# Performance work log

Measured on AMD Instinct MI355X. Metric: run time of the kernel, lower is better.

The kernel has to match this reference:

```python
import jax, jax.numpy as jnp
import numpy as np

DIM = 2048
DIM_HEAD = 64
HEADS = 16
FF_MULT = 4
LORA_R = 8
ATTN_INNER = DIM_HEAD * HEADS            # 1024
FF_INNER = DIM * FF_MULT                 # 8192
FUSED_DIMS = (ATTN_INNER, DIM_HEAD, DIM_HEAD, FF_INNER * 2)
B, N = 2, 2048


def setup_inputs() -> dict:
    key = jax.random.key(0)
    ks = jax.random.split(key, 12)
    s = 0.02
    inp = {
        "x": jax.random.normal(ks[0], (B, N, DIM), dtype=jnp.float32),
        "gamma": jnp.ones((DIM,), dtype=jnp.float32),
        "w_fused": jax.random.normal(ks[1], (DIM, sum(FUSED_DIMS)), dtype=jnp.float32) * s,
        "w_attn_out": jax.random.normal(ks[2], (ATTN_INNER, DIM), dtype=jnp.float32) * s,
        "w_ff_out": jax.random.normal(ks[3], (FF_INNER, DIM), dtype=jnp.float32) * s,
        "lora_q_a": jax.random.normal(ks[4], (DIM, LORA_R), dtype=jnp.float32) * s,
        "lora_q_b": jax.random.normal(ks[5], (LORA_R, ATTN_INNER), dtype=jnp.float32) * s,
        "lora_k_a": jax.random.normal(ks[6], (DIM, LORA_R), dtype=jnp.float32) * s,
        "lora_k_b": jax.random.normal(ks[7], (LORA_R, DIM_HEAD), dtype=jnp.float32) * s,
        "lora_v_a": jax.random.normal(ks[8], (DIM, LORA_R), dtype=jnp.float32) * s,
        "lora_v_b": jax.random.normal(ks[9], (LORA_R, DIM_HEAD), dtype=jnp.float32) * s,
        "lora_o_a": jax.random.normal(ks[10], (ATTN_INNER, LORA_R), dtype=jnp.float32) * s,
        "lora_o_b": jax.random.normal(ks[11], (LORA_R, DIM), dtype=jnp.float32) * s,
    }
    return inp


def _rotate_half(x):
    x1, x2 = jnp.split(x, 2, axis=-1)
    return jnp.concatenate((-x2, x1), axis=-1)


def _rope(pos, t):
    return t * jnp.cos(pos) + _rotate_half(t) * jnp.sin(pos)


def _forward(x, gamma, w_fused, w_attn_out, w_ff_out,
             lora_q_a, lora_q_b, lora_k_a, lora_k_b,
             lora_v_a, lora_v_b, lora_o_a, lora_o_b):
    b, n, d = x.shape
    # LayerNorm (beta = 0)
    mu = jnp.mean(x, axis=-1, keepdims=True)
    var = jnp.var(x, axis=-1, keepdims=True)
    xn = (x - mu) * jax.lax.rsqrt(var + 1e-5) * gamma

    fused = xn @ w_fused
    i0, i1, i2 = np.cumsum(FUSED_DIMS)[:3]
    q, k, v, ff = fused[..., :i0], fused[..., i0:i1], fused[..., i1:i2], fused[..., i2:]

    # LoRA additive terms
    q = q + (xn @ lora_q_a) @ lora_q_b
    k = k + (xn @ lora_k_a) @ lora_k_b
    v = v + (xn @ lora_v_a) @ lora_v_b

    q = q.reshape(b, n, HEADS, DIM_HEAD).transpose(0, 2, 1, 3)  # b h n d
    q = q * (DIM_HEAD ** -0.5)

    # rotary embedding: pos (n, dim_head)
    inv_freq = 1.0 / (10000.0 ** (jnp.arange(0, DIM_HEAD, 2, dtype=jnp.float32) / DIM_HEAD))
    freqs = jnp.arange(n, dtype=jnp.float32)[:, None] * inv_freq[None, :]
    pos = jnp.concatenate((freqs, freqs), axis=-1)
    q = _rope(pos, q)
    k = _rope(pos, k)  # k is b n d (multi-query, single kv head)

    sim = jnp.einsum('bhid,bjd->bhij', q, k)
    causal = jnp.triu(jnp.ones((n, n), dtype=bool), k=1)
    sim = jnp.where(causal, -jnp.finfo(sim.dtype).max, sim)
    attn = jax.nn.softmax(sim, axis=-1)
    out = jnp.einsum('bhij,bjd->bhid', attn, v)
    out = out.transpose(0, 2, 1, 3).reshape(b, n, ATTN_INNER)

    attn_out = out @ w_attn_out + (out @ lora_o_a) @ lora_o_b

    # SwiGLU: chunk -> (x_ff, gate); silu(gate) * x_ff
    x_ff, gate = jnp.split(ff, 2, axis=-1)
    ff_out = (jax.nn.silu(gate) * x_ff) @ w_ff_out

    return attn_out + ff_out


def reference(x, gamma, w_fused, w_attn_out, w_ff_out,
              lora_q_a, lora_q_b, lora_k_a, lora_k_b,
              lora_v_a, lora_v_b, lora_o_a, lora_o_b):
    return _forward(x, gamma, w_fused, w_attn_out, w_ff_out,
                    lora_q_a, lora_q_b, lora_k_a, lora_k_b,
                    lora_v_a, lora_v_b, lora_o_a, lora_o_b)
```

## Files before the change

kernel.cpp:

```cpp
#include <hip/hip_runtime.h>
#include <cstdint>


typedef __bf16 bf16_t;
typedef __bf16 bf16x8 __attribute__((ext_vector_type(8)));
typedef float f32x4 __attribute__((ext_vector_type(4)));

#define LOG2E 1.44269504088896340736f
#define LOG2_10K 13.287712379549449f

__device__ __forceinline__ void gload_lds16(const void* g, void* l) {
  __builtin_amdgcn_global_load_lds(
      (__attribute__((address_space(1))) void*)(uintptr_t)g,
      (__attribute__((address_space(3))) void*)(uint32_t)(uintptr_t)l,
      16, 0, 0);
}

__device__ __forceinline__ f32x4 mfma16(bf16x8 a, bf16x8 b, f32x4 c) {
  return __builtin_amdgcn_mfma_f32_16x16x32_bf16(a, b, c, 0, 0, 0);
}

__global__ __launch_bounds__(256) void ln_kernel(
    const float* __restrict__ x, const float* __restrict__ gamma,
    bf16_t* __restrict__ xn)
{
  const int row = blockIdx.x;
  const int t = threadIdx.x;
  const float4* xr = (const float4*)(x + (size_t)row * 2048);
  float4 a = xr[t * 2];
  float4 b = xr[t * 2 + 1];
  float s  = a.x + a.y + a.z + a.w + b.x + b.y + b.z + b.w;
  float ss = a.x*a.x + a.y*a.y + a.z*a.z + a.w*a.w
           + b.x*b.x + b.y*b.y + b.z*b.z + b.w*b.w;
  #pragma unroll
  for (int m = 1; m < 64; m <<= 1) {
    s  += __shfl_xor(s, m);
    ss += __shfl_xor(ss, m);
  }
  __shared__ float red[8];
  const int wave = t >> 6, lane = t & 63;
  if (lane == 0) { red[wave] = s; red[4 + wave] = ss; }
  __syncthreads();
  const float stot  = red[0] + red[1] + red[2] + red[3];
  const float sstot = red[4] + red[5] + red[6] + red[7];
  const float mu  = stot * (1.f / 2048.f);
  const float var = sstot * (1.f / 2048.f) - mu * mu;
  const float rs  = rsqrtf(var + 1e-5f);
  float v[8] = {a.x, a.y, a.z, a.w, b.x, b.y, b.z, b.w};
  bf16x8 o;
  #pragma unroll
  for (int e = 0; e < 8; ++e)
    o[e] = (bf16_t)((v[e] - mu) * rs * gamma[t * 8 + e]);
  *(bf16x8*)(xn + (size_t)row * 2048 + t * 8) = o;
}

__global__ __launch_bounds__(256) void transpose_wf_kernel(
    const float* __restrict__ w,
    const float* __restrict__ qa, const float* __restrict__ qb,
    const float* __restrict__ ka, const float* __restrict__ kb,
    const float* __restrict__ va, const float* __restrict__ vb,
    bf16_t* __restrict__ wfT)
{
  __shared__ float tile[64][65];
  const int t  = threadIdx.x;
  const int n0 = blockIdx.x * 64;
  const int k0 = blockIdx.y * 64;
  #pragma unroll
  for (int it = 0; it < 4; ++it) {
    const int kr = (t >> 4) + it * 16;
    const float4 vv = *(const float4*)(w + (size_t)(k0 + kr) * 17536 + n0 + (t & 15) * 4);
    tile[kr][(t & 15) * 4 + 0] = vv.x;
    tile[kr][(t & 15) * 4 + 1] = vv.y;
    tile[kr][(t & 15) * 4 + 2] = vv.z;
    tile[kr][(t & 15) * 4 + 3] = vv.w;
  }
  __syncthreads();
  const float* la = nullptr; const float* lb = nullptr;
  int nbo = 0, ldlb = 0;
  if (n0 < 1024)      { la = qa; lb = qb; nbo = n0;        ldlb = 1024; }
  else if (n0 < 1088) { la = ka; lb = kb; nbo = n0 - 1024; ldlb = 64;   }
  else if (n0 < 1152) { la = va; lb = vb; nbo = n0 - 1088; ldlb = 64;   }
  #pragma unroll
  for (int it = 0; it < 2; ++it) {
    const int nl = (t >> 3) + it * 32;
    const int kl = (t & 7) * 8;
    float vals[8];
    #pragma unroll
    for (int e = 0; e < 8; ++e) vals[e] = tile[kl + e][nl];
    if (la) {
      float bc[8];
      #pragma unroll
      for (int r = 0; r < 8; ++r) bc[r] = lb[r * ldlb + nbo + nl];
      #pragma unroll
      for (int e = 0; e < 8; ++e) {
        const float* ar = la + (size_t)(k0 + kl + e) * 8;
        float d = 0.f;
        #pragma unroll
        for (int r = 0; r < 8; ++r) d += ar[r] * bc[r];
        vals[e] += d;
      }
    }
    bf16x8 o;
    #pragma unroll
    for (int e = 0; e < 8; ++e) o[e] = (bf16_t)vals[e];
    *(bf16x8*)(wfT + (size_t)(n0 + nl) * 2048 + k0 + kl) = o;
  }
}

__global__ __launch_bounds__(256) void transpose_w2_kernel(
    const float* __restrict__ wff,
    const float* __restrict__ watt,
    const float* __restrict__ oa, const float* __restrict__ ob,
    bf16_t* __restrict__ w2T)
{
  __shared__ float tile[64][65];
  const int t  = threadIdx.x;
  const int n0 = blockIdx.x * 64;
  const int k0 = blockIdx.y * 64;
  const bool isatt = (k0 >= 8192);
  const float* src = isatt ? (watt + (size_t)(k0 - 8192) * 2048)
                           : (wff + (size_t)k0 * 2048);
  #pragma unroll
  for (int it = 0; it < 4; ++it) {
    const int kr = (t >> 4) + it * 16;
    const float4 vv = *(const float4*)(src + (size_t)kr * 2048 + n0 + (t & 15) * 4);
    tile[kr][(t & 15) * 4 + 0] = vv.x;
    tile[kr][(t & 15) * 4 + 1] = vv.y;
    tile[kr][(t & 15) * 4 + 2] = vv.z;
    tile[kr][(t & 15) * 4 + 3] = vv.w;
  }
  __syncthreads();
  #pragma unroll
  for (int it = 0; it < 2; ++it) {
    const int nl = (t >> 3) + it * 32;
    const int kl = (t & 7) * 8;
    float vals[8];
    #pragma unroll
    for (int e = 0; e < 8; ++e) vals[e] = tile[kl + e][nl];
    if (isatt) {
      float bc[8];
      #pragma unroll
      for (int r = 0; r < 8; ++r) bc[r] = ob[r * 2048 + n0 + nl];
      #pragma unroll
      for (int e = 0; e < 8; ++e) {
        const float* ar = oa + (size_t)(k0 - 8192 + kl + e) * 8;
        float d = 0.f;
        #pragma unroll
        for (int r = 0; r < 8; ++r) d += ar[r] * bc[r];
        vals[e] += d;
      }
    }
    bf16x8 o;
    #pragma unroll
    for (int e = 0; e < 8; ++e) o[e] = (bf16_t)vals[e];
    *(bf16x8*)(w2T + (size_t)(n0 + nl) * 9216 + k0 + kl) = o;
  }
}

__device__ __forceinline__ void gemm_core_128x128(
    const bf16_t* __restrict__ A, int ldA, int m0,
    const bf16_t* __restrict__ BT, int ldB, int n0,
    int K, bf16_t* As, bf16_t* Bs, f32x4* acc)
{
  const int t = threadIdx.x;
  const int wave = t >> 6;
  const int lane = t & 63;
  const int quad = lane >> 4;
  const int ln15 = lane & 15;
  const int wm = wave & 1, wn = wave >> 1;

  const bf16_t* gA = A + (size_t)(m0 + (t >> 2)) * ldA + ((t & 3) << 3);
  const bf16_t* gB = BT + (size_t)(n0 + (t >> 2)) * ldB + ((t & 3) << 3);
  char* lA = (char*)As + wave * 1024;
  char* lB = (char*)Bs + wave * 1024;
  const size_t sA64 = (size_t)64 * ldA;
  const size_t sB64 = (size_t)64 * ldB;
  const int aoff = (wm * 64 + ln15) * 32 + quad * 8;
  const int boff = (wn * 64 + ln15) * 32 + quad * 8;

  for (int kt = 0; kt < K; kt += 32) {
    gload_lds16(gA,        lA);
    gload_lds16(gA + sA64, lA + 4096);
    gload_lds16(gB,        lB);
    gload_lds16(gB + sB64, lB + 4096);
    gA += 32;
    gB += 32;
    __syncthreads();
    bf16x8 a0 = *(const bf16x8*)(As + aoff);
    bf16x8 a1 = *(const bf16x8*)(As + aoff + 512);
    bf16x8 a2 = *(const bf16x8*)(As + aoff + 1024);
    bf16x8 a3 = *(const bf16x8*)(As + aoff + 1536);
    bf16x8 b0 = *(const bf16x8*)(Bs + boff);
    bf16x8 b1 = *(const bf16x8*)(Bs + boff + 512);
    bf16x8 b2 = *(const bf16x8*)(Bs + boff + 1024);
    bf16x8 b3 = *(const bf16x8*)(Bs + boff + 1536);
    acc[0]  = mfma16(a0, b0, acc[0]);
    acc[1]  = mfma16(a0, b1, acc[1]);
    acc[2]  = mfma16(a0, b2, acc[2]);
    acc[3]  = mfma16(a0, b3, acc[3]);
    acc[4]  = mfma16(a1, b0, acc[4]);
    acc[5]  = mfma16(a1, b1, acc[5]);
    acc[6]  = mfma16(a1, b2, acc[6]);
    acc[7]  = mfma16(a1, b3, acc[7]);
    acc[8]  = mfma16(a2, b0, acc[8]);
    acc[9]  = mfma16(a2, b1, acc[9]);
    acc[10] = mfma16(a2, b2, acc[10]);
    acc[11] = mfma16(a2, b3, acc[11]);
    acc[12] = mfma16(a3, b0, acc[12]);
    acc[13] = mfma16(a3, b1, acc[13]);
    acc[14] = mfma16(a3, b2, acc[14]);
    acc[15] = mfma16(a3, b3, acc[15]);
    __syncthreads();
  }
}

__global__ __launch_bounds__(256) void gemm1_qkv_kernel(
    const bf16_t* __restrict__ xn, const bf16_t* __restrict__ wfT,
    bf16_t* __restrict__ Q, bf16_t* __restrict__ K, bf16_t* __restrict__ Vt)
{
  __shared__ __align__(16) bf16_t As[128 * 32];
  __shared__ __align__(16) bf16_t Bs[128 * 32];
  const int m0 = blockIdx.x * 128;
  const int ct = blockIdx.y;
  const int t = threadIdx.x;
  const int wave = t >> 6, lane = t & 63;
  const int quad = lane >> 4, ln15 = lane & 15;
  const int wm = wave & 1, wn = wave >> 1;

  f32x4 acc[16];
  #pragma unroll
  for (int f = 0; f < 16; ++f) acc[f] = (f32x4){0.f, 0.f, 0.f, 0.f};
  gemm_core_128x128(xn, 2048, m0, wfT, 2048, ct * 128, 2048, As, Bs, acc);

  const int rb = m0 + wm * 64 + quad * 4;
  const bool is_k = (ct == 8) && (wn == 0);
  const bool is_v = (ct == 8) && (wn == 1);
  const float invf0 = exp2f(-(float)ln15 * (LOG2_10K / 32.0f));
  const float invf1 = exp2f(-(float)(16 + ln15) * (LOG2_10K / 32.0f));
  const int hd = ct * 2 + wn;

  #pragma unroll
  for (int i = 0; i < 4; ++i) {
    #pragma unroll
    for (int rr = 0; rr < 4; ++rr) {
      const int row = rb + i * 16 + rr;
      const int b = row >> 11, n = row & 2047;
      float vals[4];
      #pragma unroll
      for (int j = 0; j < 4; ++j) vals[j] = acc[i * 4 + j][rr];
      if (is_v) {
        #pragma unroll
        for (int j = 0; j < 4; ++j)
          Vt[((size_t)b * 64 + j * 16 + ln15) * 2048 + n] = (bf16_t)vals[j];
      } else {
        const float fn = (float)n;
        float s0, c0, s1, c1;
        __sincosf(fn * invf0, &s0, &c0);
        __sincosf(fn * invf1, &s1, &c1);
        #pragma unroll
        for (int j = 0; j < 4; ++j) {
          const float rot = (j < 2) ? -vals[j + 2] : vals[j - 2];
          const float c = (j & 1) ? c1 : c0;
          const float s = (j & 1) ? s1 : s0;
          const float o = vals[j] * c + rot * s;
          const int d = j * 16 + ln15;
          if (is_k)
            K[((size_t)b * 2048 + n) * 64 + d] = (bf16_t)o;
          else
            Q[(((size_t)b * 16 + hd) * 2048 + n) * 64 + d] = (bf16_t)(o * 0.125f);
        }
      }
    }
  }
}

__global__ __launch_bounds__(256, 2) void gemm1_ff_kernel(
    const bf16_t* __restrict__ xn, const bf16_t* __restrict__ wfT,
    bf16_t* __restrict__ A2)
{
  __shared__ __align__(16) bf16_t As[128 * 32];
  __shared__ __align__(16) bf16_t Bg[128 * 32];
  __shared__ __align__(16) bf16_t Bx[128 * 32];
  const int m0 = blockIdx.x * 128;
  const int c  = blockIdx.y;
  const int t = threadIdx.x;
  const int wave = t >> 6, lane = t & 63;
  const int quad = lane >> 4, ln15 = lane & 15;
  const int wm = wave & 1, wn = wave >> 1;

  const bf16_t* gA = xn  + (size_t)(m0 + (t >> 2)) * 2048 + ((t & 3) << 3);
  const bf16_t* gG = wfT + (size_t)(9344 + c * 128 + (t >> 2)) * 2048 + ((t & 3) << 3);
  const bf16_t* gX = wfT + (size_t)(1152 + c * 128 + (t >> 2)) * 2048 + ((t & 3) << 3);
  char* lA = (char*)As + wave * 1024;
  char* lG = (char*)Bg + wave * 1024;
  char* lX = (char*)Bx + wave * 1024;
  const size_t s64 = (size_t)64 * 2048;
  const int aoff = (wm * 64 + ln15) * 32 + quad * 8;
  const int boff = (wn * 64 + ln15) * 32 + quad * 8;

  f32x4 accg[16], accx[16];
  #pragma unroll
  for (int f = 0; f < 16; ++f) {
    accg[f] = (f32x4){0.f, 0.f, 0.f, 0.f};
    accx[f] = (f32x4){0.f, 0.f, 0.f, 0.f};
  }

  for (int kt = 0; kt < 2048; kt += 32) {
    gload_lds16(gA,       lA);
    gload_lds16(gA + s64, lA + 4096);
    gload_lds16(gG,       lG);
    gload_lds16(gG + s64, lG + 4096);
    gload_lds16(gX,       lX);
    gload_lds16(gX + s64, lX + 4096);
    gA += 32; gG += 32; gX += 32;
    __syncthreads();
    bf16x8 a0 = *(const bf16x8*)(As + aoff);
    bf16x8 a1 = *(const bf16x8*)(As + aoff + 512);
    bf16x8 a2 = *(const bf16x8*)(As + aoff + 1024);
    bf16x8 a3 = *(const bf16x8*)(As + aoff + 1536);
    bf16x8 g0 = *(const bf16x8*)(Bg + boff);
    bf16x8 g1 = *(const bf16x8*)(Bg + boff + 512);
    bf16x8 g2 = *(const bf16x8*)(Bg + boff + 1024);
    bf16x8 g3 = *(const bf16x8*)(Bg + boff + 1536);
    bf16x8 x0 = *(const bf16x8*)(Bx + boff);
    bf16x8 x1 = *(const bf16x8*)(Bx + boff + 512);
    bf16x8 x2 = *(const bf16x8*)(Bx + boff + 1024);
    bf16x8 x3 = *(const bf16x8*)(Bx + boff + 1536);
    accg[0]  = mfma16(a0, g0, accg[0]);
    accg[1]  = mfma16(a0, g1, accg[1]);
    accg[2]  = mfma16(a0, g2, accg[2]);
    accg[3]  = mfma16(a0, g3, accg[3]);
    accx[0]  = mfma16(a0, x0, accx[0]);
    accx[1]  = mfma16(a0, x1, accx[1]);
    accx[2]  = mfma16(a0, x2, accx[2]);
    accx[3]  = mfma16(a0, x3, accx[3]);
    accg[4]  = mfma16(a1, g0, accg[4]);
    accg[5]  = mfma16(a1, g1, accg[5]);
    accg[6]  = mfma16(a1, g2, accg[6]);
    accg[7]  = mfma16(a1, g3, accg[7]);
    accx[4]  = mfma16(a1, x0, accx[4]);
    accx[5]  = mfma16(a1, x1, accx[5]);
    accx[6]  = mfma16(a1, x2, accx[6]);
    accx[7]  = mfma16(a1, x3, accx[7]);
    accg[8]  = mfma16(a2, g0, accg[8]);
    accg[9]  = mfma16(a2, g1, accg[9]);
    accg[10] = mfma16(a2, g2, accg[10]);
    accg[11] = mfma16(a2, g3, accg[11]);
    accx[8]  = mfma16(a2, x0, accx[8]);
    accx[9]  = mfma16(a2, x1, accx[9]);
    accx[10] = mfma16(a2, x2, accx[10]);
    accx[11] = mfma16(a2, x3, accx[11]);
    accg[12] = mfma16(a3, g0, accg[12]);
    accg[13] = mfma16(a3, g1, accg[13]);
    accg[14] = mfma16(a3, g2, accg[14]);
    accg[15] = mfma16(a3, g3, accg[15]);
    accx[12] = mfma16(a3, x0, accx[12]);
    accx[13] = mfma16(a3, x1, accx[13]);
    accx[14] = mfma16(a3, x2, accx[14]);
    accx[15] = mfma16(a3, x3, accx[15]);
    __syncthreads();
  }

  const int rb = m0 + wm * 64 + quad * 4;
  const int cb = c * 128 + wn * 64 + ln15;
  #pragma unroll
  for (int i = 0; i < 4; ++i)
    #pragma unroll
    for (int rr = 0; rr < 4; ++rr) {
      bf16_t* dst = A2 + (size_t)(rb + i * 16 + rr) * 9216 + cb;
      #pragma unroll
      for (int j = 0; j < 4; ++j) {
        const float g = accg[i * 4 + j][rr];
        const float xv = accx[i * 4 + j][rr];
        dst[j * 16] = (bf16_t)(xv * (g / (1.f + exp2f(-g * LOG2E))));
      }
    }
}

__global__ __launch_bounds__(256, 2) void gemm2_kernel(
    const bf16_t* __restrict__ A2, const bf16_t* __restrict__ w2T,
    float* __restrict__ out)
{
  __shared__ __align__(16) bf16_t As[128 * 32];
  __shared__ __align__(16) bf16_t B0[128 * 32];
  __shared__ __align__(16) bf16_t B1[128 * 32];
  const int m0 = blockIdx.x * 128;
  const int n0 = blockIdx.y * 256;
  const int k0 = blockIdx.z * 4608;
  const int t = threadIdx.x;
  const int wave = t >> 6, lane = t & 63;
  const int quad = lane >> 4, ln15 = lane & 15;
  const int wm = wave & 1, wn = wave >> 1;

  const bf16_t* gA  = A2  + (size_t)(m0 + (t >> 2)) * 9216 + k0 + ((t & 3) << 3);
  const bf16_t* gB0 = w2T + (size_t)(n0 + (t >> 2)) * 9216 + k0 + ((t & 3) << 3);
  const bf16_t* gB1 = w2T + (size_t)(n0 + 128 + (t >> 2)) * 9216 + k0 + ((t & 3) << 3);
  char* lA = (char*)As + wave * 1024;
  char* l0 = (char*)B0 + wave * 1024;
  char* l1 = (char*)B1 + wave * 1024;
  const size_t s64 = (size_t)64 * 9216;
  const int aoff = (wm * 64 + ln15) * 32 + quad * 8;
  const int boff = (wn * 64 + ln15) * 32 + quad * 8;

  f32x4 acc0[16], acc1[16];
  #pragma unroll
  for (int f = 0; f < 16; ++f) {
    acc0[f] = (f32x4){0.f, 0.f, 0.f, 0.f};
    acc1[f] = (f32x4){0.f, 0.f, 0.f, 0.f};
  }

  for (int kt = 0; kt < 4608; kt += 32) {
    gload_lds16(gA,        lA);
    gload_lds16(gA + s64,  lA + 4096);
    gload_lds16(gB0,       l0);
    gload_lds16(gB0 + s64, l0 + 4096);
    gload_lds16(gB1,       l1);
    gload_lds16(gB1 + s64, l1 + 4096);
    gA += 32; gB0 += 32; gB1 += 32;
    __syncthreads();
    bf16x8 a0 = *(const bf16x8*)(As + aoff);
    bf16x8 a1 = *(const bf16x8*)(As + aoff + 512);
    bf16x8 a2 = *(const bf16x8*)(As + aoff + 1024);
    bf16x8 a3 = *(const bf16x8*)(As + aoff + 1536);
    bf16x8 p0 = *(const bf16x8*)(B0 + boff);
    bf16x8 p1 = *(const bf16x8*)(B0 + boff + 512);
    bf16x8 p2 = *(const bf16x8*)(B0 + boff + 1024);
    bf16x8 p3 = *(const bf16x8*)(B0 + boff + 1536);
    bf16x8 q0 = *(const bf16x8*)(B1 + boff);
    bf16x8 q1 = *(const bf16x8*)(B1 + boff + 512);
    bf16x8 q2 = *(const bf16x8*)(B1 + boff + 1024);
    bf16x8 q3 = *(const bf16x8*)(B1 + boff + 1536);
    acc0[0]  = mfma16(a0, p0, acc0[0]);
    acc0[1]  = mfma16(a0, p1, acc0[1]);
    acc0[2]  = mfma16(a0, p2, acc0[2]);
    acc0[3]  = mfma16(a0, p3, acc0[3]);
    acc1[0]  = mfma16(a0, q0, acc1[0]);
    acc1[1]  = mfma16(a0, q1, acc1[1]);
    acc1[2]  = mfma16(a0, q2, acc1[2]);
    acc1[3]  = mfma16(a0, q3, acc1[3]);
    acc0[4]  = mfma16(a1, p0, acc0[4]);
    acc0[5]  = mfma16(a1, p1, acc0[5]);
    acc0[6]  = mfma16(a1, p2, acc0[6]);
    acc0[7]  = mfma16(a1, p3, acc0[7]);
    acc1[4]  = mfma16(a1, q0, acc1[4]);
    acc1[5]  = mfma16(a1, q1, acc1[5]);
    acc1[6]  = mfma16(a1, q2, acc1[6]);
    acc1[7]  = mfma16(a1, q3, acc1[7]);
    acc0[8]  = mfma16(a2, p0, acc0[8]);
    acc0[9]  = mfma16(a2, p1, acc0[9]);
    acc0[10] = mfma16(a2, p2, acc0[10]);
    acc0[11] = mfma16(a2, p3, acc0[11]);
    acc1[8]  = mfma16(a2, q0, acc1[8]);
    acc1[9]  = mfma16(a2, q1, acc1[9]);
    acc1[10] = mfma16(a2, q2, acc1[10]);
    acc1[11] = mfma16(a2, q3, acc1[11]);
    acc0[12] = mfma16(a3, p0, acc0[12]);
    acc0[13] = mfma16(a3, p1, acc0[13]);
    acc0[14] = mfma16(a3, p2, acc0[14]);
    acc0[15] = mfma16(a3, p3, acc0[15]);
    acc1[12] = mfma16(a3, q0, acc1[12]);
    acc1[13] = mfma16(a3, q1, acc1[13]);
    acc1[14] = mfma16(a3, q2, acc1[14]);
    acc1[15] = mfma16(a3, q3, acc1[15]);
    __syncthreads();
  }

  const int rb = m0 + wm * 64 + quad * 4;
  #pragma unroll
  for (int half = 0; half < 2; ++half) {
    const f32x4* acc = half ? acc1 : acc0;
    const int cb = n0 + half * 128 + wn * 64 + ln15;
    #pragma unroll
    for (int i = 0; i < 4; ++i)
      #pragma unroll
      for (int rr = 0; rr < 4; ++rr) {
        float* dst = out + (size_t)(rb + i * 16 + rr) * 2048 + cb;
        #pragma unroll
        for (int j = 0; j < 4; ++j)
          unsafeAtomicAdd(dst + j * 16, acc[i * 4 + j][rr]);
      }
  }
}

__global__ __launch_bounds__(256) void attn_kernel(
    const bf16_t* __restrict__ Q, const bf16_t* __restrict__ Kg_,
    const bf16_t* __restrict__ Vt, bf16_t* __restrict__ A2)
{
  __shared__ __align__(16) bf16_t Qs[128 * 64];
  __shared__ __align__(16) bf16_t Ks[64 * 64];
  __shared__ __align__(16) bf16_t Vs[64 * 64];
  __shared__ __align__(16) bf16_t Ps[128 * 64];
  const int pidx = blockIdx.x, bh = blockIdx.y;
  const int b = bh >> 4, h = bh & 15;
  const int t = threadIdx.x;
  const int wave = t >> 6, lane = t & 63;
  const int quad = lane >> 4, ln15 = lane & 15;

  const bf16_t* Kg = Kg_ + (size_t)b * 2048 * 64;
  const bf16_t* Vg = Vt + (size_t)b * 64 * 2048;

  for (int hlf = 0; hlf < 2; ++hlf) {
    const int qt = hlf ? (15 - pidx) : pidx;
    const int qm0 = qt * 128;
    const bf16_t* Qg = Q + ((size_t)bh * 2048 + qm0) * 64;

    {
      const bf16_t* g = Qg + (size_t)(t >> 3) * 64 + ((t & 7) << 3);
      char* l = (char*)Qs + wave * 1024;
      gload_lds16(g,            l);
      gload_lds16(g + 32 * 64,  l + 4096);
      gload_lds16(g + 64 * 64,  l + 8192);
      gload_lds16(g + 96 * 64,  l + 12288);
    }

    float mstate[2][4], lstate[2][4];
    f32x4 o_acc[2][4];
    #pragma unroll
    for (int i = 0; i < 2; ++i)
      #pragma unroll
      for (int rr = 0; rr < 4; ++rr) { mstate[i][rr] = -1e30f; lstate[i][rr] = 0.f; }
    #pragma unroll
    for (int i = 0; i < 2; ++i)
      #pragma unroll
      for (int jd = 0; jd < 4; ++jd) o_acc[i][jd] = (f32x4){0.f, 0.f, 0.f, 0.f};

    const int njt = qt * 2 + 2;
    for (int jt = 0; jt < njt; ++jt) {
      {
        const bf16_t* kg = Kg + (size_t)(jt * 64 + (t >> 3)) * 64 + ((t & 7) << 3);
        char* lk = (char*)Ks + wave * 1024;
        gload_lds16(kg,           lk);
        gload_lds16(kg + 32 * 64, lk + 4096);
        const bf16_t* vg = Vg + (size_t)(t >> 3) * 2048 + jt * 64 + ((t & 7) << 3);
        char* lv = (char*)Vs + wave * 1024;
        gload_lds16(vg,                   lv);
        gload_lds16(vg + (size_t)32*2048, lv + 4096);
      }
      __syncthreads();

      f32x4 sA[2][4];
      #pragma unroll
      for (int i = 0; i < 2; ++i)
        #pragma unroll
        for (int j = 0; j < 4; ++j) sA[i][j] = (f32x4){0.f, 0.f, 0.f, 0.f};
      #pragma unroll
      for (int ks = 0; ks < 2; ++ks) {
        bf16x8 aq0 = *(const bf16x8*)(Qs + (wave * 32 + ln15) * 64 + ks * 32 + quad * 8);
        bf16x8 aq1 = *(const bf16x8*)(Qs + (wave * 32 + 16 + ln15) * 64 + ks * 32 + quad * 8);
        #pragma unroll
        for (int j = 0; j < 4; ++j) {
          bf16x8 bk = *(const bf16x8*)(Ks + (j * 16 + ln15) * 64 + ks * 32 + quad * 8);
          sA[0][j] = mfma16(aq0, bk, sA[0][j]);
          sA[1][j] = mfma16(aq1, bk, sA[1][j]);
        }
      }

      const bool needmask = (jt * 64 + 63 > qm0 + wave * 32);
      #pragma unroll
      for (int i = 0; i < 2; ++i) {
        const int row0 = qm0 + wave * 32 + i * 16 + quad * 4;
        float alpha[4];
        #pragma unroll
        for (int rr = 0; rr < 4; ++rr) {
          const int rowg = row0 + rr;
          if (needmask) {
            #pragma unroll
            for (int j = 0; j < 4; ++j) {
              const int colg = jt * 64 + j * 16 + ln15;
              if (colg > rowg) sA[i][j][rr] = -1e30f;
            }
          }
          float mx = fmaxf(fmaxf(sA[i][0][rr], sA[i][1][rr]),
                           fmaxf(sA[i][2][rr], sA[i][3][rr]));
          mx = fmaxf(mx, __shfl_xor(mx, 1));
          mx = fmaxf(mx, __shfl_xor(mx, 2));
          mx = fmaxf(mx, __shfl_xor(mx, 4));
          mx = fmaxf(mx, __shfl_xor(mx, 8));
          const float mold = mstate[i][rr];
          const float mnew = fmaxf(mold, mx);
          const float al = exp2f((mold - mnew) * LOG2E);
          float rsum = 0.f;
          #pragma unroll
          for (int j = 0; j < 4; ++j) {
            const float p = exp2f((sA[i][j][rr] - mnew) * LOG2E);
            sA[i][j][rr] = p;
            rsum += p;
          }
          rsum += __shfl_xor(rsum, 1);
          rsum += __shfl_xor(rsum, 2);
          rsum += __shfl_xor(rsum, 4);
          rsum += __shfl_xor(rsum, 8);
          lstate[i][rr] = lstate[i][rr] * al + rsum;
          mstate[i][rr] = mnew;
          alpha[rr] = al;
        }
        #pragma unroll
        for (int jd = 0; jd < 4; ++jd)
          #pragma unroll
          for (int rr = 0; rr < 4; ++rr)
            o_acc[i][jd][rr] *= alpha[rr];
        #pragma unroll
        for (int j = 0; j < 4; ++j)
          #pragma unroll
          for (int rr = 0; rr < 4; ++rr)
            Ps[wave * 2048 + (i * 16 + quad * 4 + rr) * 64 + j * 16 + ln15] =
                (bf16_t)sA[i][j][rr];
      }

      #pragma unroll
      for (int ks = 0; ks < 2; ++ks) {
        bf16x8 ap0 = *(const bf16x8*)(Ps + wave * 2048 + ln15 * 64 + ks * 32 + quad * 8);
        bf16x8 ap1 = *(const bf16x8*)(Ps + wave * 2048 + (16 + ln15) * 64 + ks * 32 + quad * 8);
        #pragma unroll
        for (int jd = 0; jd < 4; ++jd) {
          bf16x8 bv = *(const bf16x8*)(Vs + (jd * 16 + ln15) * 64 + ks * 32 + quad * 8);
          o_acc[0][jd] = mfma16(ap0, bv, o_acc[0][jd]);
          o_acc[1][jd] = mfma16(ap1, bv, o_acc[1][jd]);
        }
      }
      __syncthreads();
    }

    #pragma unroll
    for (int i = 0; i < 2; ++i) {
      const int row0 = qm0 + wave * 32 + i * 16 + quad * 4;
      #pragma unroll
      for (int rr = 0; rr < 4; ++rr) {
        const float inv = 1.f / lstate[i][rr];
        bf16_t* dst = A2 + ((size_t)b * 2048 + row0 + rr) * 9216 + 8192 + h * 64 + ln15;
        #pragma unroll
        for (int jd = 0; jd < 4; ++jd)
          dst[jd * 16] = (bf16_t)(o_acc[i][jd][rr] * inv);
      }
    }
  }
}

extern "C" void kernel_launch(void* const* d_in, const int* in_sizes, int n_in,
                              void* d_out, int out_size, void* d_ws, size_t ws_size,
                              hipStream_t stream)
{
  const float* x      = (const float*)d_in[0];
  const float* gamma  = (const float*)d_in[1];
  const float* wfused = (const float*)d_in[2];
  const float* watt   = (const float*)d_in[3];
  const float* wff    = (const float*)d_in[4];
  const float* qa     = (const float*)d_in[5];
  const float* qb     = (const float*)d_in[6];
  const float* ka     = (const float*)d_in[7];
  const float* kb     = (const float*)d_in[8];
  const float* va     = (const float*)d_in[9];
  const float* vb     = (const float*)d_in[10];
  const float* oa     = (const float*)d_in[11];
  const float* ob     = (const float*)d_in[12];
  float* out = (float*)d_out;

  char* ws = (char*)d_ws;
  bf16_t* xn  = (bf16_t*)(ws);
  bf16_t* wfT = (bf16_t*)(ws + 16777216);
  bf16_t* w2T = (bf16_t*)(ws + 88604672);
  bf16_t* A2  = (bf16_t*)(ws + 126353408);
  bf16_t* Qr  = (bf16_t*)(ws + 201850880);
  bf16_t* Kr  = (bf16_t*)(ws + 210239488);
  bf16_t* Vtr = (bf16_t*)(ws + 210763776);

  hipMemsetAsync(d_out, 0, (size_t)out_size * sizeof(float), stream);

  ln_kernel<<<dim3(4096), dim3(256), 0, stream>>>(x, gamma, xn);
  transpose_wf_kernel<<<dim3(274, 32), dim3(256), 0, stream>>>(
      wfused, qa, qb, ka, kb, va, vb, wfT);
  transpose_w2_kernel<<<dim3(32, 144), dim3(256), 0, stream>>>(
      wff, watt, oa, ob, w2T);
  gemm1_qkv_kernel<<<dim3(32, 9), dim3(256), 0, stream>>>(xn, wfT, Qr, Kr, Vtr);
  gemm1_ff_kernel<<<dim3(32, 64), dim3(256), 0, stream>>>(xn, wfT, A2);
  attn_kernel<<<dim3(8, 32), dim3(256), 0, stream>>>(Qr, Kr, Vtr, A2);
  gemm2_kernel<<<dim3(32, 8, 2), dim3(256), 0, stream>>>(A2, w2T, out);
}
```

Baseline: 1.010 ms.

## Retile QKV GEMM to 128x256, shrink attention Q tile to 64, split FF launch

The Q projection blocks now compute 128x256 tiles through a shared dual-B GEMM core, cutting the QKV grid from 9 to 5 column blocks. K and V get a separate 128x128 path. The attention kernel drops from 128-row to 64-row query tiles with one 16-row slice per wave. That doubles the grid and halves LDS so two blocks can share a CU, which should improve occupancy and causal load balance. The FF GEMM is split into two launches over halves of M, and the duplicated GEMM loops are pulled into a single helper.

```diff
diff --git a/kernel.cpp b/kernel.cpp
--- a/kernel.cpp
+++ b/kernel.cpp
@@ -214,222 +214,48 @@
   }
 }
 
-__global__ __launch_bounds__(256) void gemm1_qkv_kernel(
-    const bf16_t* __restrict__ xn, const bf16_t* __restrict__ wfT,
-    bf16_t* __restrict__ Q, bf16_t* __restrict__ K, bf16_t* __restrict__ Vt)
-{
-  __shared__ __align__(16) bf16_t As[128 * 32];
-  __shared__ __align__(16) bf16_t Bs[128 * 32];
-  const int m0 = blockIdx.x * 128;
-  const int ct = blockIdx.y;
+__device__ __forceinline__ void gemm_core_dual(
+    const bf16_t* gA, const bf16_t* gB0, const bf16_t* gB1,
+    int ldA, int ldB, int K,
+    bf16_t* As, bf16_t* B0s, bf16_t* B1s,
+    f32x4* acc0, f32x4* acc1)
+{
   const int t = threadIdx.x;
-  const int wave = t >> 6, lane = t & 63;
-  const int quad = lane >> 4, ln15 = lane & 15;
+  const int wave = t >> 6;
+  const int lane = t & 63;
+  const int quad = lane >> 4;
+  const int ln15 = lane & 15;
   const int wm = wave & 1, wn = wave >> 1;
 
-  f32x4 acc[16];
-  #pragma unroll
-  for (int f = 0; f < 16; ++f) acc[f] = (f32x4){0.f, 0.f, 0.f, 0.f};
-  gemm_core_128x128(xn, 2048, m0, wfT, 2048, ct * 128, 2048, As, Bs, acc);
-
-  const int rb = m0 + wm * 64 + quad * 4;
-  const bool is_k = (ct == 8) && (wn == 0);
-  const bool is_v = (ct == 8) && (wn == 1);
-  const float invf0 = exp2f(-(float)ln15 * (LOG2_10K / 32.0f));
-  const float invf1 = exp2f(-(float)(16 + ln15) * (LOG2_10K / 32.0f));
-  const int hd = ct * 2 + wn;
-
-  #pragma unroll
-  for (int i = 0; i < 4; ++i) {
-    #pragma unroll
-    for (int rr = 0; rr < 4; ++rr) {
-      const int row = rb + i * 16 + rr;
-      const int b = row >> 11, n = row & 2047;
-      float vals[4];
-      #pragma unroll
-      for (int j = 0; j < 4; ++j) vals[j] = acc[i * 4 + j][rr];
-      if (is_v) {
-        #pragma unroll
-        for (int j = 0; j < 4; ++j)
-          Vt[((size_t)b * 64 + j * 16 + ln15) * 2048 + n] = (bf16_t)vals[j];
-      } else {
-        const float fn = (float)n;
-        float s0, c0, s1, c1;
-        __sincosf(fn * invf0, &s0, &c0);
-        __sincosf(fn * invf1, &s1, &c1);
-        #pragma unroll
-        for (int j = 0; j < 4; ++j) {
-          const float rot = (j < 2) ? -vals[j + 2] : vals[j - 2];
-          const float c = (j & 1) ? c1 : c0;
-          const float s = (j & 1) ? s1 : s0;
-          const float o = vals[j] * c + rot * s;
-          const int d = j * 16 + ln15;
-          if (is_k)
-            K[((size_t)b * 2048 + n) * 64 + d] = (bf16_t)o;
-          else
-            Q[(((size_t)b * 16 + hd) * 2048 + n) * 64 + d] = (bf16_t)(o * 0.125f);
-        }
-      }
-    }
-  }
-}
-
-__global__ __launch_bounds__(256, 2) void gemm1_ff_kernel(
-    const bf16_t* __restrict__ xn, const bf16_t* __restrict__ wfT,
-    bf16_t* __restrict__ A2)
-{
-  __shared__ __align__(16) bf16_t As[128 * 32];
-  __shared__ __align__(16) bf16_t Bg[128 * 32];
-  __shared__ __align__(16) bf16_t Bx[128 * 32];
-  const int m0 = blockIdx.x * 128;
-  const int c  = blockIdx.y;
-  const int t = threadIdx.x;
-  const int wave = t >> 6, lane = t & 63;
-  const int quad = lane >> 4, ln15 = lane & 15;
-  const int wm = wave & 1, wn = wave >> 1;
-
-  const bf16_t* gA = xn  + (size_t)(m0 + (t >> 2)) * 2048 + ((t & 3) << 3);
-  const bf16_t* gG = wfT + (size_t)(9344 + c * 128 + (t >> 2)) * 2048 + ((t & 3) << 3);
-  const bf16_t* gX = wfT + (size_t)(1152 + c * 128 + (t >> 2)) * 2048 + ((t & 3) << 3);
   char* lA = (char*)As + wave * 1024;
-  char* lG = (char*)Bg + wave * 1024;
-  char* lX = (char*)Bx + wave * 1024;
-  const size_t s64 = (size_t)64 * 2048;
+  char* l0 = (char*)B0s + wave * 1024;
+  char* l1 = (char*)B1s + wave * 1024;
+  const size_t sA64 = (size_t)64 * ldA;
+  const size_t sB64 = (size_t)64 * ldB;
   const int aoff = (wm * 64 + ln15) * 32 + quad * 8;
   const int boff = (wn * 64 + ln15) * 32 + quad * 8;
 
-  f32x4 accg[16], accx[16];
-  #pragma unroll
-  for (int f = 0; f < 16; ++f) {
-    accg[f] = (f32x4){0.f, 0.f, 0.f, 0.f};
-    accx[f] = (f32x4){0.f, 0.f, 0.f, 0.f};
-  }
-
-  for (int kt = 0; kt < 2048; kt += 32) {
-    gload_lds16(gA,       lA);
-    gload_lds16(gA + s64, lA + 4096);
-    gload_lds16(gG,       lG);
-    gload_lds16(gG + s64, lG + 4096);
-    gload_lds16(gX,       lX);
-    gload_lds16(gX + s64, lX + 4096);
-    gA += 32; gG += 32; gX += 32;
-    __syncthreads();
-    bf16x8 a0 = *(const bf16x8*)(As + aoff);
-    bf16x8 a1 = *(const bf16x8*)(As + aoff + 512);
-    bf16x8 a2 = *(const bf16x8*)(As + aoff + 1024);
-    bf16x8 a3 = *(const bf16x8*)(As + aoff + 1536);
-    bf16x8 g0 = *(const bf16x8*)(Bg + boff);
-    bf16x8 g1 = *(const bf16x8*)(Bg + boff + 512);
-    bf16x8 g2 = *(const bf16x8*)(Bg + boff + 1024);
-    bf16x8 g3 = *(const bf16x8*)(Bg + boff + 1536);
-    bf16x8 x0 = *(const bf16x8*)(Bx + boff);
-    bf16x8 x1 = *(const bf16x8*)(Bx + boff + 512);
-    bf16x8 x2 = *(const bf16x8*)(Bx + boff + 1024);
-    bf16x8 x3 = *(const bf16x8*)(Bx + boff + 1536);
-    accg[0]  = mfma16(a0, g0, accg[0]);
-    accg[1]  = mfma16(a0, g1, accg[1]);
-    accg[2]  = mfma16(a0, g2, accg[2]);
-    accg[3]  = mfma16(a0, g3, accg[3]);
-    accx[0]  = mfma16(a0, x0, accx[0]);
-    accx[1]  = mfma16(a0, x1, accx[1]);
-    accx[2]  = mfma16(a0, x2, accx[2]);
-    accx[3]  = mfma16(a0, x3, accx[3]);
-    accg[4]  = mfma16(a1, g0, accg[4]);
-    accg[5]  = mfma16(a1, g1, accg[5]);
-    accg[6]  = mfma16(a1, g2, accg[6]);
-    accg[7]  = mfma16(a1, g3, accg[7]);
-    accx[4]  = mfma16(a1, x0, accx[4]);
-    accx[5]  = mfma16(a1, x1, accx[5]);
-    accx[6]  = mfma16(a1, x2, accx[6]);
-    accx[7]  = mfma16(a1, x3, accx[7]);
-    accg[8]  = mfma16(a2, g0, accg[8]);
-    accg[9]  = mfma16(a2, g1, accg[9]);
-    accg[10] = mfma16(a2, g2, accg[10]);
-    accg[11] = mfma16(a2, g3, accg[11]);
-    accx[8]  = mfma16(a2, x0, accx[8]);
-    accx[9]  = mfma16(a2, x1, accx[9]);
-    accx[10] = mfma16(a2, x2, accx[10]);
-    accx[11] = mfma16(a2, x3, accx[11]);
-    accg[12] = mfma16(a3, g0, accg[12]);
-    accg[13] = mfma16(a3, g1, accg[13]);
-    accg[14] = mfma16(a3, g2, accg[14]);
-    accg[15] = mfma16(a3, g3, accg[15]);
-    accx[12] = mfma16(a3, x0, accx[12]);
-    accx[13] = mfma16(a3, x1, accx[13]);
-    accx[14] = mfma16(a3, x2, accx[14]);
-    accx[15] = mfma16(a3, x3, accx[15]);
-    __syncthreads();
-  }
-
-  const int rb = m0 + wm * 64 + quad * 4;
-  const int cb = c * 128 + wn * 64 + ln15;
-  #pragma unroll
-  for (int i = 0; i < 4; ++i)
-    #pragma unroll
-    for (int rr = 0; rr < 4; ++rr) {
-      bf16_t* dst = A2 + (size_t)(rb + i * 16 + rr) * 9216 + cb;
-      #pragma unroll
-      for (int j = 0; j < 4; ++j) {
-        const float g = accg[i * 4 + j][rr];
-        const float xv = accx[i * 4 + j][rr];
-        dst[j * 16] = (bf16_t)(xv * (g / (1.f + exp2f(-g * LOG2E))));
-      }
-    }
-}
-
-__global__ __launch_bounds__(256, 2) void gemm2_kernel(
-    const bf16_t* __restrict__ A2, const bf16_t* __restrict__ w2T,
-    float* __restrict__ out)
-{
-  __shared__ __align__(16) bf16_t As[128 * 32];
-  __shared__ __align__(16) bf16_t B0[128 * 32];
-  __shared__ __align__(16) bf16_t B1[128 * 32];
-  const int m0 = blockIdx.x * 128;
-  const int n0 = blockIdx.y * 256;
-  const int k0 = blockIdx.z * 4608;
-  const int t = threadIdx.x;
-  const int wave = t >> 6, lane = t & 63;
-  const int quad = lane >> 4, ln15 = lane & 15;
-  const int wm = wave & 1, wn = wave >> 1;
-
-  const bf16_t* gA  = A2  + (size_t)(m0 + (t >> 2)) * 9216 + k0 + ((t & 3) << 3);
-  const bf16_t* gB0 = w2T + (size_t)(n0 + (t >> 2)) * 9216 + k0 + ((t & 3) << 3);
-  const bf16_t* gB1 = w2T + (size_t)(n0 + 128 + (t >> 2)) * 9216 + k0 + ((t & 3) << 3);
-  char* lA = (char*)As + wave * 1024;
-  char* l0 = (char*)B0 + wave * 1024;
-  char* l1 = (char*)B1 + wave * 1024;
-  const size_t s64 = (size_t)64 * 9216;
-  const int aoff = (wm * 64 + ln15) * 32 + quad * 8;
-  const int boff = (wn * 64 + ln15) * 32 + quad * 8;
-
-  f32x4 acc0[16], acc1[16];
-  #pragma unroll
-  for (int f = 0; f < 16; ++f) {
-    acc0[f] = (f32x4){0.f, 0.f, 0.f, 0.f};
-    acc1[f] = (f32x4){0.f, 0.f, 0.f, 0.f};
-  }
-
-  for (int kt = 0; kt < 4608; kt += 32) {
-    gload_lds16(gA,        lA);
-    gload_lds16(gA + s64,  lA + 4096);
-    gload_lds16(gB0,       l0);
-    gload_lds16(gB0 + s64, l0 + 4096);
-    gload_lds16(gB1,       l1);
-    gload_lds16(gB1 + s64, l1 + 4096);
+  for (int kt = 0; kt < K; kt += 32) {
+    gload_lds16(gA,         lA);
+    gload_lds16(gA + sA64,  lA + 4096);
+    gload_lds16(gB0,        l0);
+    gload_lds16(gB0 + sB64, l0 + 4096);
+    gload_lds16(gB1,        l1);
+    gload_lds16(gB1 + sB64, l1 + 4096);
     gA += 32; gB0 += 32; gB1 += 32;
     __syncthreads();
     bf16x8 a0 = *(const bf16x8*)(As + aoff);
     bf16x8 a1 = *(const bf16x8*)(As + aoff + 512);
     bf16x8 a2 = *(const bf16x8*)(As + aoff + 1024);
     bf16x8 a3 = *(const bf16x8*)(As + aoff + 1536);
-    bf16x8 p0 = *(const bf16x8*)(B0 + boff);
-    bf16x8 p1 = *(const bf16x8*)(B0 + boff + 512);
-    bf16x8 p2 = *(const bf16x8*)(B0 + boff + 1024);
-    bf16x8 p3 = *(const bf16x8*)(B0 + boff + 1536);
-    bf16x8 q0 = *(const bf16x8*)(B1 + boff);
-    bf16x8 q1 = *(const bf16x8*)(B1 + boff + 512);
-    bf16x8 q2 = *(const bf16x8*)(B1 + boff + 1024);
-    bf16x8 q3 = *(const bf16x8*)(B1 + boff + 1536);
+    bf16x8 p0 = *(const bf16x8*)(B0s + boff);
+    bf16x8 p1 = *(const bf16x8*)(B0s + boff + 512);
+    bf16x8 p2 = *(const bf16x8*)(B0s + boff + 1024);
+    bf16x8 p3 = *(const bf16x8*)(B0s + boff + 1536);
+    bf16x8 q0 = *(const bf16x8*)(B1s + boff);
+    bf16x8 q1 = *(const bf16x8*)(B1s + boff + 512);
+    bf16x8 q2 = *(const bf16x8*)(B1s + boff + 1024);
+    bf16x8 q3 = *(const bf16x8*)(B1s + boff + 1536);
     acc0[0]  = mfma16(a0, p0, acc0[0]);
     acc0[1]  = mfma16(a0, p1, acc0[1]);
     acc0[2]  = mfma16(a0, p2, acc0[2]);
@@ -464,6 +290,170 @@
     acc1[15] = mfma16(a3, q3, acc1[15]);
     __syncthreads();
   }
+}
+
+__global__ __launch_bounds__(256, 2) void gemm1_qkv_kernel(
+    const bf16_t* __restrict__ xn, const bf16_t* __restrict__ wfT,
+    bf16_t* __restrict__ Q, bf16_t* __restrict__ K, bf16_t* __restrict__ Vt)
+{
+  __shared__ __align__(16) bf16_t As[128 * 32];
+  __shared__ __align__(16) bf16_t B0s[128 * 32];
+  __shared__ __align__(16) bf16_t B1s[128 * 32];
+  const int m0 = blockIdx.x * 128;
+  const int y = blockIdx.y;
+  const int t = threadIdx.x;
+  const int wave = t >> 6, lane = t & 63;
+  const int quad = lane >> 4, ln15 = lane & 15;
+  const int wm = wave & 1, wn = wave >> 1;
+
+  const int rb = m0 + wm * 64 + quad * 4;
+  const float invf0 = exp2f(-(float)ln15 * (LOG2_10K / 32.0f));
+  const float invf1 = exp2f(-(float)(16 + ln15) * (LOG2_10K / 32.0f));
+
+  if (y < 4) {
+    const bf16_t* gA  = xn  + (size_t)(m0 + (t >> 2)) * 2048 + ((t & 3) << 3);
+    const bf16_t* gB0 = wfT + (size_t)(y * 256 + (t >> 2)) * 2048 + ((t & 3) << 3);
+    const bf16_t* gB1 = wfT + (size_t)(y * 256 + 128 + (t >> 2)) * 2048 + ((t & 3) << 3);
+    f32x4 acc0[16], acc1[16];
+    #pragma unroll
+    for (int f = 0; f < 16; ++f) {
+      acc0[f] = (f32x4){0.f, 0.f, 0.f, 0.f};
+      acc1[f] = (f32x4){0.f, 0.f, 0.f, 0.f};
+    }
+    gemm_core_dual(gA, gB0, gB1, 2048, 2048, 2048, As, B0s, B1s, acc0, acc1);
+    #pragma unroll
+    for (int half = 0; half < 2; ++half) {
+      const f32x4* acc = half ? acc1 : acc0;
+      const int hd = y * 4 + half * 2 + wn;
+      #pragma unroll
+      for (int i = 0; i < 4; ++i) {
+        #pragma unroll
+        for (int rr = 0; rr < 4; ++rr) {
+          const int row = rb + i * 16 + rr;
+          const int b = row >> 11, n = row & 2047;
+          const float fn = (float)n;
+          float s0, c0, s1, c1;
+          __sincosf(fn * invf0, &s0, &c0);
+          __sincosf(fn * invf1, &s1, &c1);
+          float vals[4];
+          #pragma unroll
+          for (int j = 0; j < 4; ++j) vals[j] = acc[i * 4 + j][rr];
+          #pragma unroll
+          for (int j = 0; j < 4; ++j) {
+            const float rot = (j < 2) ? -vals[j + 2] : vals[j - 2];
+            const float c = (j & 1) ? c1 : c0;
+            const float s = (j & 1) ? s1 : s0;
+            const float o = (vals[j] * c + rot * s) * 0.125f;
+            Q[(((size_t)b * 16 + hd) * 2048 + n) * 64 + j * 16 + ln15] = (bf16_t)o;
+          }
+        }
+      }
+    }
+  } else {
+    f32x4 acc[16];
+    #pragma unroll
+    for (int f = 0; f < 16; ++f) acc[f] = (f32x4){0.f, 0.f, 0.f, 0.f};
+    gemm_core_128x128(xn, 2048, m0, wfT, 2048, 1024, 2048, As, B0s, acc);
+    const bool is_k = (wn == 0);
+    #pragma unroll
+    for (int i = 0; i < 4; ++i) {
+      #pragma unroll
+      for (int rr = 0; rr < 4; ++rr) {
+        const int row = rb + i * 16 + rr;
+        const int b = row >> 11, n = row & 2047;
+        float vals[4];
+        #pragma unroll
+        for (int j = 0; j < 4; ++j) vals[j] = acc[i * 4 + j][rr];
+        if (is_k) {
+          const float fn = (float)n;
+          float s0, c0, s1, c1;
+          __sincosf(fn * invf0, &s0, &c0);
+          __sincosf(fn * invf1, &s1, &c1);
+          #pragma unroll
+          for (int j = 0; j < 4; ++j) {
+            const float rot = (j < 2) ? -vals[j + 2] : vals[j - 2];
+            const float c = (j & 1) ? c1 : c0;
+            const float s = (j & 1) ? s1 : s0;
+            K[((size_t)b * 2048 + n) * 64 + j * 16 + ln15] = (bf16_t)(vals[j] * c + rot * s);
+          }
+        } else {
+          #pragma unroll
+          for (int j = 0; j < 4; ++j)
+            Vt[((size_t)b * 64 + j * 16 + ln15) * 2048 + n] = (bf16_t)vals[j];
+        }
+      }
+    }
+  }
+}
+
+__global__ __launch_bounds__(256, 2) void gemm1_ff_kernel(
+    const bf16_t* __restrict__ xn, const bf16_t* __restrict__ wfT,
+    bf16_t* __restrict__ A2, int m_base)
+{
+  __shared__ __align__(16) bf16_t As[128 * 32];
+  __shared__ __align__(16) bf16_t Bg[128 * 32];
+  __shared__ __align__(16) bf16_t Bx[128 * 32];
+  const int m0 = m_base + blockIdx.x * 128;
+  const int c  = blockIdx.y;
+  const int t = threadIdx.x;
+  const int wave = t >> 6, lane = t & 63;
+  const int quad = lane >> 4, ln15 = lane & 15;
+  const int wm = wave & 1, wn = wave >> 1;
+
+  const bf16_t* gA = xn  + (size_t)(m0 + (t >> 2)) * 2048 + ((t & 3) << 3);
+  const bf16_t* gG = wfT + (size_t)(9344 + c * 128 + (t >> 2)) * 2048 + ((t & 3) << 3);
+  const bf16_t* gX = wfT + (size_t)(1152 + c * 128 + (t >> 2)) * 2048 + ((t & 3) << 3);
+
+  f32x4 accg[16], accx[16];
+  #pragma unroll
+  for (int f = 0; f < 16; ++f) {
+    accg[f] = (f32x4){0.f, 0.f, 0.f, 0.f};
+    accx[f] = (f32x4){0.f, 0.f, 0.f, 0.f};
+  }
+  gemm_core_dual(gA, gG, gX, 2048, 2048, 2048, As, Bg, Bx, accg, accx);
+
+  const int rb = m0 + wm * 64 + quad * 4;
+  const int cb = c * 128 + wn * 64 + ln15;
+  #pragma unroll
+  for (int i = 0; i < 4; ++i)
+    #pragma unroll
+    for (int rr = 0; rr < 4; ++rr) {
+      bf16_t* dst = A2 + (size_t)(rb + i * 16 + rr) * 9216 + cb;
+      #pragma unroll
+      for (int j = 0; j < 4; ++j) {
+        const float g = accg[i * 4 + j][rr];
+        const float xv = accx[i * 4 + j][rr];
+        dst[j * 16] = (bf16_t)(xv * (g / (1.f + exp2f(-g * LOG2E))));
+      }
+    }
+}
+
+__global__ __launch_bounds__(256, 2) void gemm2_kernel(
+    const bf16_t* __restrict__ A2, const bf16_t* __restrict__ w2T,
+    float* __restrict__ out)
+{
+  __shared__ __align__(16) bf16_t As[128 * 32];
+  __shared__ __align__(16) bf16_t B0[128 * 32];
+  __shared__ __align__(16) bf16_t B1[128 * 32];
+  const int m0 = blockIdx.x * 128;
+  const int n0 = blockIdx.y * 256;
+  const int k0 = blockIdx.z * 4608;
+  const int t = threadIdx.x;
+  const int wave = t >> 6, lane = t & 63;
+  const int quad = lane >> 4, ln15 = lane & 15;
+  const int wm = wave & 1, wn = wave >> 1;
+
+  const bf16_t* gA  = A2  + (size_t)(m0 + (t >> 2)) * 9216 + k0 + ((t & 3) << 3);
+  const bf16_t* gB0 = w2T + (size_t)(n0 + (t >> 2)) * 9216 + k0 + ((t & 3) << 3);
+  const bf16_t* gB1 = w2T + (size_t)(n0 + 128 + (t >> 2)) * 9216 + k0 + ((t & 3) << 3);
+
+  f32x4 acc0[16], acc1[16];
+  #pragma unroll
+  for (int f = 0; f < 16; ++f) {
+    acc0[f] = (f32x4){0.f, 0.f, 0.f, 0.f};
+    acc1[f] = (f32x4){0.f, 0.f, 0.f, 0.f};
+  }
+  gemm_core_dual(gA, gB0, gB1, 9216, 9216, 4608, As, B0, B1, acc0, acc1);
 
   const int rb = m0 + wm * 64 + quad * 4;
   #pragma unroll
@@ -482,14 +472,14 @@
   }
 }
 
-__global__ __launch_bounds__(256) void attn_kernel(
+__global__ __launch_bounds__(256, 2) void attn_kernel(
     const bf16_t* __restrict__ Q, const bf16_t* __restrict__ Kg_,
     const bf16_t* __restrict__ Vt, bf16_t* __restrict__ A2)
 {
-  __shared__ __align__(16) bf16_t Qs[128 * 64];
+  __shared__ __align__(16) bf16_t Qs[64 * 64];
   __shared__ __align__(16) bf16_t Ks[64 * 64];
   __shared__ __align__(16) bf16_t Vs[64 * 64];
-  __shared__ __align__(16) bf16_t Ps[128 * 64];
+  __shared__ __align__(16) bf16_t Ps[64 * 64];
   const int pidx = blockIdx.x, bh = blockIdx.y;
   const int b = bh >> 4, h = bh & 15;
   const int t = threadIdx.x;
@@ -500,31 +490,25 @@
   const bf16_t* Vg = Vt + (size_t)b * 64 * 2048;
 
   for (int hlf = 0; hlf < 2; ++hlf) {
-    const int qt = hlf ? (15 - pidx) : pidx;
-    const int qm0 = qt * 128;
+    const int qt = hlf ? (31 - pidx) : pidx;
+    const int qm0 = qt * 64;
     const bf16_t* Qg = Q + ((size_t)bh * 2048 + qm0) * 64;
 
     {
       const bf16_t* g = Qg + (size_t)(t >> 3) * 64 + ((t & 7) << 3);
       char* l = (char*)Qs + wave * 1024;
-      gload_lds16(g,            l);
-      gload_lds16(g + 32 * 64,  l + 4096);
-      gload_lds16(g + 64 * 64,  l + 8192);
-      gload_lds16(g + 96 * 64,  l + 12288);
-    }
-
-    float mstate[2][4], lstate[2][4];
-    f32x4 o_acc[2][4];
-    #pragma unroll
-    for (int i = 0; i < 2; ++i)
-      #pragma unroll
-      for (int rr = 0; rr < 4; ++rr) { mstate[i][rr] = -1e30f; lstate[i][rr] = 0.f; }
-    #pragma unroll
-    for (int i = 0; i < 2; ++i)
-      #pragma unroll
-      for (int jd = 0; jd < 4; ++jd) o_acc[i][jd] = (f32x4){0.f, 0.f, 0.f, 0.f};
-
-    const int njt = qt * 2 + 2;
+      gload_lds16(g,           l);
+      gload_lds16(g + 32 * 64, l + 4096);
+    }
+
+    float mstate[4], lstate[4];
+    f32x4 o_acc[4];
+    #pragma unroll
+    for (int rr = 0; rr < 4; ++rr) { mstate[rr] = -1e30f; lstate[rr] = 0.f; }
+    #pragma unroll
+    for (int jd = 0; jd < 4; ++jd) o_acc[jd] = (f32x4){0.f, 0.f, 0.f, 0.f};
+
+    const int njt = qt + 1;
     for (int jt = 0; jt < njt; ++jt) {
       {
         const bf16_t* kg = Kg + (size_t)(jt * 64 + (t >> 3)) * 64 + ((t & 7) << 3);
@@ -538,100 +522,87 @@
       }
       __syncthreads();
 
-      f32x4 sA[2][4];
-      #pragma unroll
-      for (int i = 0; i < 2; ++i)
-        #pragma unroll
-        for (int j = 0; j < 4; ++j) sA[i][j] = (f32x4){0.f, 0.f, 0.f, 0.f};
+      f32x4 sA[4];
+      #pragma unroll
+      for (int j = 0; j < 4; ++j) sA[j] = (f32x4){0.f, 0.f, 0.f, 0.f};
       #pragma unroll
       for (int ks = 0; ks < 2; ++ks) {
-        bf16x8 aq0 = *(const bf16x8*)(Qs + (wave * 32 + ln15) * 64 + ks * 32 + quad * 8);
-        bf16x8 aq1 = *(const bf16x8*)(Qs + (wave * 32 + 16 + ln15) * 64 + ks * 32 + quad * 8);
+        bf16x8 aq = *(const bf16x8*)(Qs + (wave * 16 + ln15) * 64 + ks * 32 + quad * 8);
         #pragma unroll
         for (int j = 0; j < 4; ++j) {
           bf16x8 bk = *(const bf16x8*)(Ks + (j * 16 + ln15) * 64 + ks * 32 + quad * 8);
-          sA[0][j] = mfma16(aq0, bk, sA[0][j]);
-          sA[1][j] = mfma16(aq1, bk, sA[1][j]);
+          sA[j] = mfma16(aq, bk, sA[j]);
         }
       }
 
-      const bool needmask = (jt * 64 + 63 > qm0 + wave * 32);
-      #pragma unroll
-      for (int i = 0; i < 2; ++i) {
-        const int row0 = qm0 + wave * 32 + i * 16 + quad * 4;
-        float alpha[4];
-        #pragma unroll
-        for (int rr = 0; rr < 4; ++rr) {
-          const int rowg = row0 + rr;
-          if (needmask) {
-            #pragma unroll
-            for (int j = 0; j < 4; ++j) {
-              const int colg = jt * 64 + j * 16 + ln15;
-              if (colg > rowg) sA[i][j][rr] = -1e30f;
-            }
-          }
-          float mx = fmaxf(fmaxf(sA[i][0][rr], sA[i][1][rr]),
-                           fmaxf(sA[i][2][rr], sA[i][3][rr]));
-          mx = fmaxf(mx, __shfl_xor(mx, 1));
-          mx = fmaxf(mx, __shfl_xor(mx, 2));
-          mx = fmaxf(mx, __shfl_xor(mx, 4));
-          mx = fmaxf(mx, __shfl_xor(mx, 8));
-          const float mold = mstate[i][rr];
-          const float mnew = fmaxf(mold, mx);
-          const float al = exp2f((mold - mnew) * LOG2E);
-          float rsum = 0.f;
+      const bool needmask = (jt * 64 + 63 > qm0 + wave * 16);
+      const int row0 = qm0 + wave * 16 + quad * 4;
+      float alpha[4];
+      #pragma unroll
+      for (int rr = 0; rr < 4; ++rr) {
+        const int rowg = row0 + rr;
+        if (needmask) {
           #pragma unroll
           for (int j = 0; j < 4; ++j) {
-            const float p = exp2f((sA[i][j][rr] - mnew) * LOG2E);
-            sA[i][j][rr] = p;
-            rsum += p;
+            const int colg = jt * 64 + j * 16 + ln15;
+            if (colg > rowg) sA[j][rr] = -1e30f;
           }
-          rsum += __shfl_xor(rsum, 1);
-          rsum += __shfl_xor(rsum, 2);
-          rsum += __shfl_xor(rsum, 4);
-          rsum += __shfl_xor(rsum, 8);
-          lstate[i][rr] = lstate[i][rr] * al + rsum;
-          mstate[i][rr] = mnew;
-          alpha[rr] = al;
         }
-        #pragma unroll
-        for (int jd = 0; jd < 4; ++jd)
-          #pragma unroll
-          for (int rr = 0; rr < 4; ++rr)
-            o_acc[i][jd][rr] *= alpha[rr];
-        #pragma unroll
-        for (int j = 0; j < 4; ++j)
-          #pragma unroll
-          for (int rr = 0; rr < 4; ++rr)
-            Ps[wave * 2048 + (i * 16 + quad * 4 + rr) * 64 + j * 16 + ln15] =
-                (bf16_t)sA[i][j][rr];
-      }
+        float mx = fmaxf(fmaxf(sA[0][rr], sA[1][rr]),
+                         fmaxf(sA[2][rr], sA[3][rr]));
+        mx = fmaxf(mx, __shfl_xor(mx, 1));
+        mx = fmaxf(mx, __shfl_xor(mx, 2));
+        mx = fmaxf(mx, __shfl_xor(mx, 4));
+        mx = fmaxf(mx, __shfl_xor(mx, 8));
+        const float mold = mstate[rr];
+        const float mnew = fmaxf(mold, mx);
+        const float al = exp2f((mold - mnew) * LOG2E);
+        float rsum = 0.f;
+        #pragma unroll
+        for (int j = 0; j < 4; ++j) {
+          const float p = exp2f((sA[j][rr] - mnew) * LOG2E);
+          sA[j][rr] = p;
+          rsum += p;
+        }
+        rsum += __shfl_xor(rsum, 1);
+        rsum += __shfl_xor(rsum, 2);
+        rsum += __shfl_xor(rsum, 4);
+        rsum += __shfl_xor(rsum, 8);
+        lstate[rr] = lstate[rr] * al + rsum;
+        mstate[rr] = mnew;
+        alpha[rr] = al;
+      }
+      #pragma unroll
+      for (int jd = 0; jd < 4; ++jd)
+        #pragma unroll
+        for (int rr = 0; rr < 4; ++rr)
+          o_acc[jd][rr] *= alpha[rr];
+      #pragma unroll
+      for (int j = 0; j < 4; ++j)
+        #pragma unroll
+        for (int rr = 0; rr < 4; ++rr)
+          Ps[wave * 1024 + (quad * 4 + rr) * 64 + j * 16 + ln15] = (bf16_t)sA[j][rr];
 
       #pragma unroll
       for (int ks = 0; ks < 2; ++ks) {
-        bf16x8 ap0 = *(const bf16x8*)(Ps + wave * 2048 + ln15 * 64 + ks * 32 + quad * 8);
-        bf16x8 ap1 = *(const bf16x8*)(Ps + wave * 2048 + (16 + ln15) * 64 + ks * 32 + quad * 8);
+        bf16x8 ap = *(const bf16x8*)(Ps + wave * 1024 + ln15 * 64 + ks * 32 + quad * 8);
         #pragma unroll
         for (int jd = 0; jd < 4; ++jd) {
           bf16x8 bv = *(const bf16x8*)(Vs + (jd * 16 + ln15) * 64 + ks * 32 + quad * 8);
-          o_acc[0][jd] = mfma16(ap0, bv, o_acc[0][jd]);
-          o_acc[1][jd] = mfma16(ap1, bv, o_acc[1][jd]);
+          o_acc[jd] = mfma16(ap, bv, o_acc[jd]);
         }
       }
       __syncthreads();
     }
 
-    #pragma unroll
-    for (int i = 0; i < 2; ++i) {
-      const int row0 = qm0 + wave * 32 + i * 16 + quad * 4;
-      #pragma unroll
-      for (int rr = 0; rr < 4; ++rr) {
-        const float inv = 1.f / lstate[i][rr];
-        bf16_t* dst = A2 + ((size_t)b * 2048 + row0 + rr) * 9216 + 8192 + h * 64 + ln15;
-        #pragma unroll
-        for (int jd = 0; jd < 4; ++jd)
-          dst[jd * 16] = (bf16_t)(o_acc[i][jd][rr] * inv);
-      }
+    const int row0 = qm0 + wave * 16 + quad * 4;
+    #pragma unroll
+    for (int rr = 0; rr < 4; ++rr) {
+      const float inv = 1.f / lstate[rr];
+      bf16_t* dst = A2 + ((size_t)b * 2048 + row0 + rr) * 9216 + 8192 + h * 64 + ln15;
+      #pragma unroll
+      for (int jd = 0; jd < 4; ++jd)
+        dst[jd * 16] = (bf16_t)(o_acc[jd][rr] * inv);
     }
   }
 }
@@ -671,8 +642,9 @@
       wfused, qa, qb, ka, kb, va, vb, wfT);
   transpose_w2_kernel<<<dim3(32, 144), dim3(256), 0, stream>>>(
       wff, watt, oa, ob, w2T);
-  gemm1_qkv_kernel<<<dim3(32, 9), dim3(256), 0, stream>>>(xn, wfT, Qr, Kr, Vtr);
-  gemm1_ff_kernel<<<dim3(32, 64), dim3(256), 0, stream>>>(xn, wfT, A2);
-  attn_kernel<<<dim3(8, 32), dim3(256), 0, stream>>>(Qr, Kr, Vtr, A2);
+  gemm1_qkv_kernel<<<dim3(32, 5), dim3(256), 0, stream>>>(xn, wfT, Qr, Kr, Vtr);
+  gemm1_ff_kernel<<<dim3(16, 64), dim3(256), 0, stream>>>(xn, wfT, A2, 0);
+  gemm1_ff_kernel<<<dim3(16, 64), dim3(256), 0, stream>>>(xn, wfT, A2, 2048);
+  attn_kernel<<<dim3(16, 32), dim3(256), 0, stream>>>(Qr, Kr, Vtr, A2);
   gemm2_kernel<<<dim3(32, 8, 2), dim3(256), 0, stream>>>(A2, w2T, out);
 }
```

Result: faster. 967.4 us (-4.2%).
